# Performance work log

Measured on AMD Instinct MI355X. Metric: run time of the kernel, lower is better.

## Reference

```python
import jax, jax.numpy as jnp
import numpy as np
from jax import lax

T, H, F, E, K = 4096, 1024, 2048, 8, 2

def setup_inputs() -> dict:
    key = jax.random.key(0)
    k1, k2, k3, k4 = jax.random.split(key, 4)
    return {
        "hidden_states": jax.random.normal(k1, (T, H), jnp.float32),
        "gate_w": jax.random.normal(k2, (E, H), jnp.float32) * 0.02,
        "w1": jax.random.normal(k3, (E, 2 * F, H), jnp.float32) * 0.02,  # fused gate+up
        "w2": jax.random.normal(k4, (E, H, F), jnp.float32) * 0.02,      # down proj
        "top_k": K,
    }

def reference(hidden_states, gate_w, w1, w2, top_k):
    tokens = hidden_states.shape[0]
    # Router gate (Linear, no bias)
    router_logits = hidden_states @ gate_w.T                     # [T, E]
    probs = jax.nn.softmax(router_logits.astype(jnp.float32), axis=-1)
    topk_w, topk_idx = lax.top_k(probs, top_k)                   # [T, K]
    topk_w = topk_w / jnp.sum(topk_w, axis=-1, keepdims=True)    # renormalize
    # Dense combine weights [T, E] (zero for unselected experts)
    combine = jnp.zeros_like(probs).at[jnp.arange(tokens)[:, None], topk_idx].add(topk_w)
    combine = combine.astype(hidden_states.dtype)

    def expert_step(acc, ew):
        w1_e, w2_e, c_e = ew                                     # [2F,H], [H,F], [T]
        h = hidden_states @ w1_e.T                               # [T, 2F]
        g, u = jnp.split(h, 2, axis=-1)
        y = (jax.nn.silu(g) * u) @ w2_e.T                        # [T, H]
        return acc + c_e[:, None] * y, None

    acc0 = jnp.zeros_like(hidden_states)
    final_hidden_states, _ = lax.scan(expert_step, acc0, (w1, w2, combine.T))
    return final_hidden_states, router_logits
```

## Files before the change

### kernel.cpp

```cpp
#include <hip/hip_runtime.h>

#define T 4096
#define Hdim 1024
#define Fdim 2048
#define NE 8
#define TOPK 2
#define TK (T*TOPK)

typedef unsigned short ushort_t;
typedef __attribute__((ext_vector_type(8))) short bf16x8;
typedef __attribute__((ext_vector_type(4))) float floatx4;

__device__ __forceinline__ ushort_t f2bf(float f) {
    unsigned u = __float_as_uint(f);
    u += 0x7fff + ((u >> 16) & 1);
    return (ushort_t)(u >> 16);
}
__device__ __forceinline__ uint4 cvt8(const float4 a, const float4 b) {
    uint4 r;
    r.x = (unsigned)f2bf(a.x) | ((unsigned)f2bf(a.y) << 16);
    r.y = (unsigned)f2bf(a.z) | ((unsigned)f2bf(a.w) << 16);
    r.z = (unsigned)f2bf(b.x) | ((unsigned)f2bf(b.y) << 16);
    r.w = (unsigned)f2bf(b.z) | ((unsigned)f2bf(b.w) << 16);
    return r;
}
__device__ __forceinline__ void gld16(const ushort_t* g, short* l) {
    __builtin_amdgcn_global_load_lds((const __attribute__((address_space(1))) void*)g,
                                     (__attribute__((address_space(3))) void*)l, 16, 0, 0);
}

__global__ __launch_bounds__(256) void cvt_kernel(const float* __restrict__ src,
                                                  ushort_t* __restrict__ dst)
{
    long i = (long)blockIdx.x * 256 + threadIdx.x;
    float4 a = *(const float4*)(src + i * 8);
    float4 b = *(const float4*)(src + i * 8 + 4);
    *(uint4*)(dst + i * 8) = cvt8(a, b);
}

__global__ __launch_bounds__(64) void router_kernel(
    const float* __restrict__ hs, const float* __restrict__ gw,
    float* __restrict__ logits_out, ushort_t* __restrict__ hsb,
    int2* __restrict__ choice, float2* __restrict__ cwt, int* __restrict__ counts)
{
    const int t = blockIdx.x;
    const int lane = threadIdx.x;
    if (t == 0 && lane < NE) counts[lane] = 0;

    float hreg[16];
#pragma unroll
    for (int i = 0; i < 16; ++i)
        hreg[i] = hs[(long)t * Hdim + lane + 64 * i];

#pragma unroll
    for (int i = 0; i < 16; ++i)
        hsb[(long)t * Hdim + lane + 64 * i] = f2bf(hreg[i]);

    float acc[NE];
#pragma unroll
    for (int e = 0; e < NE; ++e) {
        float s = 0.f;
#pragma unroll
        for (int i = 0; i < 16; ++i)
            s += hreg[i] * gw[e * Hdim + lane + 64 * i];
#pragma unroll
        for (int off = 32; off > 0; off >>= 1)
            s += __shfl_xor(s, off, 64);
        acc[e] = s;
    }

    if (lane < NE) logits_out[t * NE + lane] = acc[lane];

    if (lane == 0) {
        int i1 = 0;
#pragma unroll
        for (int e = 1; e < NE; ++e) if (acc[e] > acc[i1]) i1 = e;
        int i2 = -1;
#pragma unroll
        for (int e = 0; e < NE; ++e) {
            if (e == i1) continue;
            if (i2 < 0 || acc[e] > acc[i2]) i2 = e;
        }
        float p2 = __expf(acc[i2] - acc[i1]);
        float z  = 1.f + p2;
        choice[t] = make_int2(i1, i2);
        cwt[t]    = make_float2(1.f / z, p2 / z);
    }
}

__global__ __launch_bounds__(256) void scatter_kernel(
    const int2* __restrict__ choice, const float2* __restrict__ cwt,
    int* __restrict__ counts, int* __restrict__ tok_slot, float* __restrict__ tok_wt)
{
    __shared__ int lhist[NE];
    __shared__ int lbase[NE];
    __shared__ int lpos[NE];
    const int tid = threadIdx.x;
    if (tid < NE) { lhist[tid] = 0; lpos[tid] = 0; }
    __syncthreads();

    const int t = blockIdx.x * 256 + tid;
    int2   ch = choice[t];
    float2 wv = cwt[t];
    atomicAdd(&lhist[ch.x], 1);
    atomicAdd(&lhist[ch.y], 1);
    __syncthreads();

    if (tid < NE) lbase[tid] = atomicAdd(&counts[tid], lhist[tid]);
    __syncthreads();

    int p1 = atomicAdd(&lpos[ch.x], 1);
    int p2 = atomicAdd(&lpos[ch.y], 1);
    int o1 = lbase[ch.x] + p1;
    int o2 = lbase[ch.y] + p2;
    tok_slot[ch.x * T + o1] = t * TOPK + 0;
    tok_wt [ch.x * T + o1] = wv.x;
    tok_slot[ch.y * T + o2] = t * TOPK + 1;
    tok_wt [ch.y * T + o2] = wv.y;
}

__global__ __launch_bounds__(512) void gemm1_kernel(
    const ushort_t* __restrict__ hsb, const ushort_t* __restrict__ w1b,
    const int* __restrict__ counts, const int* __restrict__ tok_slot,
    ushort_t* __restrict__ actb)
{
    const int e = blockIdx.z;
    const int cnt = counts[e];
    const int row0 = blockIdx.y * 256;
    if (row0 >= cnt) return;
    const int f0 = blockIdx.x * 128;

    __shared__ short As[2][256 * 64];
    __shared__ short Bs[2][256 * 64];
    __shared__ int slotLds[256];

    const int tid = threadIdx.x;
    if (tid < 256) {
        int idx = row0 + tid;
        slotLds[tid] = (idx < cnt) ? tok_slot[e * T + idx] : -1;
    }
    __syncthreads();

    const ushort_t* srcA[4];
    const ushort_t* srcB[4];
#pragma unroll
    for (int i = 0; i < 4; ++i) {
        int ci = i * 512 + tid;
        int r  = ci >> 3;
        int gc = (ci & 7) ^ (r & 7);
        int s  = slotLds[r];
        srcA[i] = hsb + (long)(s >= 0 ? (s >> 1) : 0) * Hdim + gc * 8;
        long frow = (r < 128) ? (long)(f0 + r) : (long)(Fdim + f0 + (r - 128));
        srcB[i] = w1b + ((long)e * 2 * Fdim + frow) * Hdim + gc * 8;
    }

    const int lane = tid & 63;
    const int w = tid >> 6;
    const int wm = (w >> 1) * 64;
    const int fn = (w & 1) * 64;
    const int fr = lane & 15, fg = lane >> 4;
    const int cs0 = (fg ^ (fr & 7)) * 8;
    const int cs1 = ((4 + fg) ^ (fr & 7)) * 8;

    floatx4 accg[4][4] = {};
    floatx4 accu[4][4] = {};

#pragma unroll
    for (int i = 0; i < 4; ++i) {
        gld16(srcA[i], &As[0][(i * 512 + tid) * 8]);
        gld16(srcB[i], &Bs[0][(i * 512 + tid) * 8]);
    }
    __syncthreads();

    const int NT = Hdim / 64;
    for (int t = 0; t < NT; ++t) {
        short* Ac = As[t & 1];
        short* Bc = Bs[t & 1];
        short* An = As[(t & 1) ^ 1];
        short* Bn = Bs[(t & 1) ^ 1];
        const bool pf = (t + 1 < NT);
        const long k1 = (long)(t + 1) * 64;

        bf16x8 a[4], b[4];

#pragma unroll
        for (int ms = 0; ms < 4; ++ms)
            a[ms] = *(const bf16x8*)&Ac[(wm + ms * 16 + fr) * 64 + cs0];
#pragma unroll
        for (int ns = 0; ns < 4; ++ns)
            b[ns] = *(const bf16x8*)&Bc[(fn + ns * 16 + fr) * 64 + cs0];
        if (pf) {
            gld16(srcA[0] + k1, &An[(0 * 512 + tid) * 8]);
            gld16(srcB[0] + k1, &Bn[(0 * 512 + tid) * 8]);
        }
        __builtin_amdgcn_s_barrier();
        __builtin_amdgcn_s_setprio(1);
#pragma unroll
        for (int ms = 0; ms < 4; ++ms)
#pragma unroll
            for (int ns = 0; ns < 4; ++ns)
                accg[ms][ns] = __builtin_amdgcn_mfma_f32_16x16x32_bf16(a[ms], b[ns], accg[ms][ns], 0, 0, 0);
        __builtin_amdgcn_s_setprio(0);
        __builtin_amdgcn_s_barrier();

#pragma unroll
        for (int ns = 0; ns < 4; ++ns)
            b[ns] = *(const bf16x8*)&Bc[(128 + fn + ns * 16 + fr) * 64 + cs0];
        if (pf) {
            gld16(srcA[1] + k1, &An[(1 * 512 + tid) * 8]);
            gld16(srcB[1] + k1, &Bn[(1 * 512 + tid) * 8]);
        }
        __builtin_amdgcn_s_barrier();
        __builtin_amdgcn_s_setprio(1);
#pragma unroll
        for (int ms = 0; ms < 4; ++ms)
#pragma unroll
            for (int ns = 0; ns < 4; ++ns)
                accu[ms][ns] = __builtin_amdgcn_mfma_f32_16x16x32_bf16(a[ms], b[ns], accu[ms][ns], 0, 0, 0);
        __builtin_amdgcn_s_setprio(0);
        __builtin_amdgcn_s_barrier();

#pragma unroll
        for (int ms = 0; ms < 4; ++ms)
            a[ms] = *(const bf16x8*)&Ac[(wm + ms * 16 + fr) * 64 + cs1];
#pragma unroll
        for (int ns = 0; ns < 4; ++ns)
            b[ns] = *(const bf16x8*)&Bc[(fn + ns * 16 + fr) * 64 + cs1];
        if (pf) {
            gld16(srcA[2] + k1, &An[(2 * 512 + tid) * 8]);
            gld16(srcB[2] + k1, &Bn[(2 * 512 + tid) * 8]);
        }
        __builtin_amdgcn_s_barrier();
        __builtin_amdgcn_s_setprio(1);
#pragma unroll
        for (int ms = 0; ms < 4; ++ms)
#pragma unroll
            for (int ns = 0; ns < 4; ++ns)
                accg[ms][ns] = __builtin_amdgcn_mfma_f32_16x16x32_bf16(a[ms], b[ns], accg[ms][ns], 0, 0, 0);
        __builtin_amdgcn_s_setprio(0);
        __builtin_amdgcn_s_barrier();

#pragma unroll
        for (int ns = 0; ns < 4; ++ns)
            b[ns] = *(const bf16x8*)&Bc[(128 + fn + ns * 16 + fr) * 64 + cs1];
        if (pf) {
            gld16(srcA[3] + k1, &An[(3 * 512 + tid) * 8]);
            gld16(srcB[3] + k1, &Bn[(3 * 512 + tid) * 8]);
        }
        __builtin_amdgcn_s_barrier();
        __builtin_amdgcn_s_setprio(1);
#pragma unroll
        for (int ms = 0; ms < 4; ++ms)
#pragma unroll
            for (int ns = 0; ns < 4; ++ns)
                accu[ms][ns] = __builtin_amdgcn_mfma_f32_16x16x32_bf16(a[ms], b[ns], accu[ms][ns], 0, 0, 0);
        __builtin_amdgcn_s_setprio(0);
        __builtin_amdgcn_sched_barrier(0);
        asm volatile("s_waitcnt vmcnt(0)" ::: "memory");
        __builtin_amdgcn_s_barrier();
    }

#pragma unroll
    for (int ms = 0; ms < 4; ++ms)
#pragma unroll
        for (int ns = 0; ns < 4; ++ns)
#pragma unroll
            for (int j = 0; j < 4; ++j) {
                int m = wm + ms * 16 + fg * 4 + j;
                int slot = slotLds[m];
                if (slot >= 0) {
                    int fcol = f0 + fn + ns * 16 + fr;
                    float gv = accg[ms][ns][j];
                    float uv = accu[ms][ns][j];
                    float av = (gv / (1.f + __expf(-gv))) * uv;
                    actb[(long)slot * Fdim + fcol] = f2bf(av);
                }
            }
}

__global__ __launch_bounds__(512) void gemm2_kernel(
    const ushort_t* __restrict__ actb, const ushort_t* __restrict__ w2b,
    const int* __restrict__ counts, const int* __restrict__ tok_slot,
    const float* __restrict__ tok_wt, float* __restrict__ partial)
{
    const int e = blockIdx.z;
    const int cnt = counts[e];
    const int row0 = blockIdx.y * 128;
    if (row0 >= cnt) return;
    const int h0 = blockIdx.x * 128;

    __shared__ short As[128 * 64];
    __shared__ short Bs[128 * 64];
    __shared__ int   slotLds[128];
    __shared__ float wtLds[128];

    const int tid = threadIdx.x;
    if (tid < 128) {
        int idx = row0 + tid;
        bool ok = idx < cnt;
        slotLds[tid] = ok ? tok_slot[e * T + idx] : -1;
        wtLds[tid]   = ok ? tok_wt [e * T + idx] : 0.f;
    }
    __syncthreads();

    const ushort_t* srcA[2];
    const ushort_t* srcB[2];
#pragma unroll
    for (int i = 0; i < 2; ++i) {
        int ci = i * 512 + tid;
        int r  = ci >> 3;
        int gc = (ci & 7) ^ (r & 7);
        int s  = slotLds[r];
        srcA[i] = actb + (long)(s >= 0 ? s : 0) * Fdim + gc * 8;
        srcB[i] = w2b + ((long)e * Hdim + (h0 + r)) * Fdim + gc * 8;
    }

    const int lane = tid & 63;
    const int w = tid >> 6;
    const int wm = (w >> 2) * 64;
    const int wn = (w & 3) * 32;
    const int fr = lane & 15, fg = lane >> 4;
    const int cs0 = (fg ^ (fr & 7)) * 8;
    const int cs1 = ((4 + fg) ^ (fr & 7)) * 8;

    floatx4 acc[4][2] = {};

    for (int k0 = 0; k0 < Fdim; k0 += 64) {
        __syncthreads();
        gld16(srcA[0] + k0, &As[tid * 8]);
        gld16(srcA[1] + k0, &As[(512 + tid) * 8]);
        gld16(srcB[0] + k0, &Bs[tid * 8]);
        gld16(srcB[1] + k0, &Bs[(512 + tid) * 8]);
        __syncthreads();

#pragma unroll
        for (int kk = 0; kk < 2; ++kk) {
            const int cs = kk ? cs1 : cs0;
            bf16x8 a[4], b[2];
#pragma unroll
            for (int ms = 0; ms < 4; ++ms)
                a[ms] = *(bf16x8*)&As[(wm + ms * 16 + fr) * 64 + cs];
#pragma unroll
            for (int ns = 0; ns < 2; ++ns)
                b[ns] = *(bf16x8*)&Bs[(wn + ns * 16 + fr) * 64 + cs];
#pragma unroll
            for (int ms = 0; ms < 4; ++ms)
#pragma unroll
                for (int ns = 0; ns < 2; ++ns)
                    acc[ms][ns] = __builtin_amdgcn_mfma_f32_16x16x32_bf16(a[ms], b[ns], acc[ms][ns], 0, 0, 0);
        }
    }

#pragma unroll
    for (int ms = 0; ms < 4; ++ms)
#pragma unroll
        for (int ns = 0; ns < 2; ++ns)
#pragma unroll
            for (int j = 0; j < 4; ++j) {
                int m = wm + ms * 16 + fg * 4 + j;
                int slot = slotLds[m];
                if (slot >= 0) {
                    int hcol = h0 + wn + ns * 16 + fr;
                    partial[(long)slot * Hdim + hcol] = acc[ms][ns][j] * wtLds[m];
                }
            }
}

__global__ __launch_bounds__(256) void combine_kernel(
    const float* __restrict__ partial, float* __restrict__ out)
{
    long i = (long)blockIdx.x * 256 + threadIdx.x;
    int t  = (int)(i / (Hdim / 4));
    int h4 = (int)(i % (Hdim / 4));
    const float4 p0 = *(const float4*)&partial[(long)(2 * t    ) * Hdim + h4 * 4];
    const float4 p1 = *(const float4*)&partial[(long)(2 * t + 1) * Hdim + h4 * 4];
    float4 s;
    s.x = p0.x + p1.x; s.y = p0.y + p1.y; s.z = p0.z + p1.z; s.w = p0.w + p1.w;
    *(float4*)&out[(long)t * Hdim + h4 * 4] = s;
}

extern "C" void kernel_launch(void* const* d_in, const int* in_sizes, int n_in,
                              void* d_out, int out_size, void* d_ws, size_t ws_size,
                              hipStream_t stream)
{
    const float* hs = (const float*)d_in[0];
    const float* gw = (const float*)d_in[1];
    const float* w1 = (const float*)d_in[2];
    const float* w2 = (const float*)d_in[3];

    float* out        = (float*)d_out;
    float* logits_out = out + (long)T * Hdim;

    char* ws = (char*)d_ws;
    size_t off = 0;
    int* counts = (int*)(ws + off);          off += 256;
    int* tok_slot = (int*)(ws + off);        off += (size_t)NE * T * sizeof(int);
    float* tok_wt = (float*)(ws + off);      off += (size_t)NE * T * sizeof(float);
    off = (off + 255) & ~(size_t)255;
    ushort_t* hsb = (ushort_t*)(ws + off);   off += (size_t)T * Hdim * sizeof(ushort_t);
    off = (off + 255) & ~(size_t)255;
    char* w1region = ws + off;               off += (size_t)NE * 2 * Fdim * Hdim * sizeof(ushort_t);
    ushort_t* w1b = (ushort_t*)w1region;
    ushort_t* w2b = (ushort_t*)w1region;
    float* partial = (float*)(w1region + (size_t)NE * Hdim * Fdim * sizeof(ushort_t));
    off = (off + 255) & ~(size_t)255;
    ushort_t* actb = (ushort_t*)(ws + off);  off += (size_t)TK * Fdim * sizeof(ushort_t);
    int2*   choice = (int2*)actb;
    float2* cwt    = (float2*)((char*)actb + (size_t)T * sizeof(int2));

    const long n8_w1 = (long)NE * 2 * Fdim * Hdim / 8;
    const long n8_w2 = (long)NE * Hdim * Fdim / 8;

    cvt_kernel<<<(int)(n8_w1 / 256), 256, 0, stream>>>(w1, w1b);
    router_kernel<<<T, 64, 0, stream>>>(hs, gw, logits_out, hsb, choice, cwt, counts);
    scatter_kernel<<<T / 256, 256, 0, stream>>>(choice, cwt, counts, tok_slot, tok_wt);
    gemm1_kernel<<<dim3(Fdim / 128, T / 256, NE), 512, 0, stream>>>(hsb, w1b, counts, tok_slot, actb);
    cvt_kernel<<<(int)(n8_w2 / 256), 256, 0, stream>>>(w2, w2b);
    gemm2_kernel<<<dim3(Hdim / 128, T / 128, NE), 512, 0, stream>>>(actb, w2b, counts, tok_slot, tok_wt, partial);
    combine_kernel<<<(int)((long)T * Hdim / 4 / 256), 256, 0, stream>>>(partial, out);
}
```

Baseline: 429.7 us.

## Triple-buffer gemm2 with 256-row tiles and regroup gemm1 prefetch waits

gemm2 moves from a single-buffered 128x128 tile with two full barriers per K step to a 256x128 tile with a three-stage LDS ring. Loads are issued two steps ahead and waited on with partial vmcnt counts, so global latency overlaps MFMA work and each B tile is reused across more rows. gemm1's prefetch is regrouped so all A loads go out in the first phase and all B loads in the second, with fine-grained vmcnt waits replacing the full drain at the end of each iteration. The cost is more LDS (about 144 KB in gemm2), which lowers occupancy, and correctness now depends on the hand-counted vmcnt values.

```diff
diff --git a/kernel.cpp b/kernel.cpp
--- a/kernel.cpp
+++ b/kernel.cpp
@@ -166,11 +166,11 @@
     floatx4 accu[4][4] = {};
 
 #pragma unroll
-    for (int i = 0; i < 4; ++i) {
-        gld16(srcA[i], &As[0][(i * 512 + tid) * 8]);
-        gld16(srcB[i], &Bs[0][(i * 512 + tid) * 8]);
-    }
-    __syncthreads();
+    for (int i = 0; i < 4; ++i) gld16(srcA[i], &As[0][(i * 512 + tid) * 8]);
+#pragma unroll
+    for (int i = 0; i < 4; ++i) gld16(srcB[i], &Bs[0][(i * 512 + tid) * 8]);
+    asm volatile("s_waitcnt vmcnt(2)" ::: "memory");
+    __builtin_amdgcn_s_barrier();
 
     const int NT = Hdim / 64;
     for (int t = 0; t < NT; ++t) {
@@ -190,8 +190,9 @@
         for (int ns = 0; ns < 4; ++ns)
             b[ns] = *(const bf16x8*)&Bc[(fn + ns * 16 + fr) * 64 + cs0];
         if (pf) {
-            gld16(srcA[0] + k1, &An[(0 * 512 + tid) * 8]);
-            gld16(srcB[0] + k1, &Bn[(0 * 512 + tid) * 8]);
+#pragma unroll
+            for (int i = 0; i < 4; ++i)
+                gld16(srcA[i] + k1, &An[(i * 512 + tid) * 8]);
         }
         __builtin_amdgcn_s_barrier();
         __builtin_amdgcn_s_setprio(1);
@@ -201,14 +202,17 @@
             for (int ns = 0; ns < 4; ++ns)
                 accg[ms][ns] = __builtin_amdgcn_mfma_f32_16x16x32_bf16(a[ms], b[ns], accg[ms][ns], 0, 0, 0);
         __builtin_amdgcn_s_setprio(0);
+        if (pf) asm volatile("s_waitcnt vmcnt(4)" ::: "memory");
+        else    asm volatile("s_waitcnt vmcnt(0)" ::: "memory");
         __builtin_amdgcn_s_barrier();
 
 #pragma unroll
         for (int ns = 0; ns < 4; ++ns)
             b[ns] = *(const bf16x8*)&Bc[(128 + fn + ns * 16 + fr) * 64 + cs0];
         if (pf) {
-            gld16(srcA[1] + k1, &An[(1 * 512 + tid) * 8]);
-            gld16(srcB[1] + k1, &Bn[(1 * 512 + tid) * 8]);
+#pragma unroll
+            for (int i = 0; i < 4; ++i)
+                gld16(srcB[i] + k1, &Bn[(i * 512 + tid) * 8]);
         }
         __builtin_amdgcn_s_barrier();
         __builtin_amdgcn_s_setprio(1);
@@ -226,10 +230,6 @@
 #pragma unroll
         for (int ns = 0; ns < 4; ++ns)
             b[ns] = *(const bf16x8*)&Bc[(fn + ns * 16 + fr) * 64 + cs1];
-        if (pf) {
-            gld16(srcA[2] + k1, &An[(2 * 512 + tid) * 8]);
-            gld16(srcB[2] + k1, &Bn[(2 * 512 + tid) * 8]);
-        }
         __builtin_amdgcn_s_barrier();
         __builtin_amdgcn_s_setprio(1);
 #pragma unroll
@@ -243,10 +243,6 @@
 #pragma unroll
         for (int ns = 0; ns < 4; ++ns)
             b[ns] = *(const bf16x8*)&Bc[(128 + fn + ns * 16 + fr) * 64 + cs1];
-        if (pf) {
-            gld16(srcA[3] + k1, &An[(3 * 512 + tid) * 8]);
-            gld16(srcB[3] + k1, &Bn[(3 * 512 + tid) * 8]);
-        }
         __builtin_amdgcn_s_barrier();
         __builtin_amdgcn_s_setprio(1);
 #pragma unroll
@@ -255,8 +251,7 @@
             for (int ns = 0; ns < 4; ++ns)
                 accu[ms][ns] = __builtin_amdgcn_mfma_f32_16x16x32_bf16(a[ms], b[ns], accu[ms][ns], 0, 0, 0);
         __builtin_amdgcn_s_setprio(0);
-        __builtin_amdgcn_sched_barrier(0);
-        asm volatile("s_waitcnt vmcnt(0)" ::: "memory");
+        if (pf) asm volatile("s_waitcnt vmcnt(2)" ::: "memory");
         __builtin_amdgcn_s_barrier();
     }
 
@@ -285,17 +280,17 @@
 {
     const int e = blockIdx.z;
     const int cnt = counts[e];
-    const int row0 = blockIdx.y * 128;
+    const int row0 = blockIdx.y * 256;
     if (row0 >= cnt) return;
     const int h0 = blockIdx.x * 128;
 
-    __shared__ short As[128 * 64];
-    __shared__ short Bs[128 * 64];
-    __shared__ int   slotLds[128];
-    __shared__ float wtLds[128];
+    __shared__ short As[3][256 * 64];
+    __shared__ short Bs[3][128 * 64];
+    __shared__ int   slotLds[256];
+    __shared__ float wtLds[256];
 
     const int tid = threadIdx.x;
-    if (tid < 128) {
+    if (tid < 256) {
         int idx = row0 + tid;
         bool ok = idx < cnt;
         slotLds[tid] = ok ? tok_slot[e * T + idx] : -1;
@@ -303,58 +298,111 @@
     }
     __syncthreads();
 
-    const ushort_t* srcA[2];
+    const ushort_t* srcA[4];
     const ushort_t* srcB[2];
 #pragma unroll
-    for (int i = 0; i < 2; ++i) {
+    for (int i = 0; i < 4; ++i) {
         int ci = i * 512 + tid;
         int r  = ci >> 3;
         int gc = (ci & 7) ^ (r & 7);
         int s  = slotLds[r];
         srcA[i] = actb + (long)(s >= 0 ? s : 0) * Fdim + gc * 8;
+    }
+#pragma unroll
+    for (int i = 0; i < 2; ++i) {
+        int ci = i * 512 + tid;
+        int r  = ci >> 3;
+        int gc = (ci & 7) ^ (r & 7);
         srcB[i] = w2b + ((long)e * Hdim + (h0 + r)) * Fdim + gc * 8;
     }
 
     const int lane = tid & 63;
     const int w = tid >> 6;
-    const int wm = (w >> 2) * 64;
-    const int wn = (w & 3) * 32;
+    const int wm = (w >> 1) * 64;
+    const int wn = (w & 1) * 64;
     const int fr = lane & 15, fg = lane >> 4;
     const int cs0 = (fg ^ (fr & 7)) * 8;
     const int cs1 = ((4 + fg) ^ (fr & 7)) * 8;
 
-    floatx4 acc[4][2] = {};
-
-    for (int k0 = 0; k0 < Fdim; k0 += 64) {
-        __syncthreads();
-        gld16(srcA[0] + k0, &As[tid * 8]);
-        gld16(srcA[1] + k0, &As[(512 + tid) * 8]);
-        gld16(srcB[0] + k0, &Bs[tid * 8]);
-        gld16(srcB[1] + k0, &Bs[(512 + tid) * 8]);
-        __syncthreads();
-
-#pragma unroll
-        for (int kk = 0; kk < 2; ++kk) {
-            const int cs = kk ? cs1 : cs0;
-            bf16x8 a[4], b[2];
-#pragma unroll
-            for (int ms = 0; ms < 4; ++ms)
-                a[ms] = *(bf16x8*)&As[(wm + ms * 16 + fr) * 64 + cs];
-#pragma unroll
-            for (int ns = 0; ns < 2; ++ns)
-                b[ns] = *(bf16x8*)&Bs[(wn + ns * 16 + fr) * 64 + cs];
-#pragma unroll
-            for (int ms = 0; ms < 4; ++ms)
-#pragma unroll
-                for (int ns = 0; ns < 2; ++ns)
-                    acc[ms][ns] = __builtin_amdgcn_mfma_f32_16x16x32_bf16(a[ms], b[ns], acc[ms][ns], 0, 0, 0);
-        }
+    floatx4 acc[4][4] = {};
+
+#pragma unroll
+    for (int i = 0; i < 4; ++i) gld16(srcA[i],      &As[0][(i * 512 + tid) * 8]);
+#pragma unroll
+    for (int i = 0; i < 2; ++i) gld16(srcB[i],      &Bs[0][(i * 512 + tid) * 8]);
+#pragma unroll
+    for (int i = 0; i < 4; ++i) gld16(srcA[i] + 64, &As[1][(i * 512 + tid) * 8]);
+#pragma unroll
+    for (int i = 0; i < 2; ++i) gld16(srcB[i] + 64, &Bs[1][(i * 512 + tid) * 8]);
+    asm volatile("s_waitcnt vmcnt(6)" ::: "memory");
+    __builtin_amdgcn_s_barrier();
+
+    const int NT = Fdim / 64;
+    int cur = 0;
+    for (int t = 0; t < NT; ++t) {
+        short* Ac = &As[cur][0];
+        short* Bc = &Bs[cur][0];
+        int stg = cur + 2; if (stg >= 3) stg -= 3;
+        short* Astg = &As[stg][0];
+        short* Bstg = &Bs[stg][0];
+        const bool pf2 = (t + 2 < NT);
+        const long k2 = (long)(t + 2) * 64;
+
+        bf16x8 a[4], b[4];
+
+#pragma unroll
+        for (int ms = 0; ms < 4; ++ms)
+            a[ms] = *(const bf16x8*)&Ac[(wm + ms * 16 + fr) * 64 + cs0];
+#pragma unroll
+        for (int ns = 0; ns < 4; ++ns)
+            b[ns] = *(const bf16x8*)&Bc[(wn + ns * 16 + fr) * 64 + cs0];
+        if (pf2) {
+#pragma unroll
+            for (int i = 0; i < 4; ++i)
+                gld16(srcA[i] + k2, &Astg[(i * 512 + tid) * 8]);
+        }
+        __builtin_amdgcn_s_barrier();
+        __builtin_amdgcn_s_setprio(1);
+#pragma unroll
+        for (int ms = 0; ms < 4; ++ms)
+#pragma unroll
+            for (int ns = 0; ns < 4; ++ns)
+                acc[ms][ns] = __builtin_amdgcn_mfma_f32_16x16x32_bf16(a[ms], b[ns], acc[ms][ns], 0, 0, 0);
+        __builtin_amdgcn_s_setprio(0);
+        __builtin_amdgcn_s_barrier();
+
+#pragma unroll
+        for (int ms = 0; ms < 4; ++ms)
+            a[ms] = *(const bf16x8*)&Ac[(wm + ms * 16 + fr) * 64 + cs1];
+#pragma unroll
+        for (int ns = 0; ns < 4; ++ns)
+            b[ns] = *(const bf16x8*)&Bc[(wn + ns * 16 + fr) * 64 + cs1];
+        if (pf2) {
+#pragma unroll
+            for (int i = 0; i < 2; ++i)
+                gld16(srcB[i] + k2, &Bstg[(i * 512 + tid) * 8]);
+        }
+        __builtin_amdgcn_s_barrier();
+        __builtin_amdgcn_s_setprio(1);
+#pragma unroll
+        for (int ms = 0; ms < 4; ++ms)
+#pragma unroll
+            for (int ns = 0; ns < 4; ++ns)
+                acc[ms][ns] = __builtin_amdgcn_mfma_f32_16x16x32_bf16(a[ms], b[ns], acc[ms][ns], 0, 0, 0);
+        __builtin_amdgcn_s_setprio(0);
+        if (t + 1 < NT) {
+            if (pf2) asm volatile("s_waitcnt vmcnt(6)" ::: "memory");
+            else     asm volatile("s_waitcnt vmcnt(0)" ::: "memory");
+        }
+        __builtin_amdgcn_s_barrier();
+
+        cur += 1; if (cur >= 3) cur -= 3;
     }
 
 #pragma unroll
     for (int ms = 0; ms < 4; ++ms)
 #pragma unroll
-        for (int ns = 0; ns < 2; ++ns)
+        for (int ns = 0; ns < 4; ++ns)
 #pragma unroll
             for (int j = 0; j < 4; ++j) {
                 int m = wm + ms * 16 + fg * 4 + j;
@@ -416,6 +464,6 @@
     scatter_kernel<<<T / 256, 256, 0, stream>>>(choice, cwt, counts, tok_slot, tok_wt);
     gemm1_kernel<<<dim3(Fdim / 128, T / 256, NE), 512, 0, stream>>>(hsb, w1b, counts, tok_slot, actb);
     cvt_kernel<<<(int)(n8_w2 / 256), 256, 0, stream>>>(w2, w2b);
-    gemm2_kernel<<<dim3(Hdim / 128, T / 128, NE), 512, 0, stream>>>(actb, w2b, counts, tok_slot, tok_wt, partial);
+    gemm2_kernel<<<dim3(Hdim / 128, T / 256, NE), 512, 0, stream>>>(actb, w2b, counts, tok_slot, tok_wt, partial);
     combine_kernel<<<(int)((long)T * Hdim / 4 / 256), 256, 0, stream>>>(partial, out);
 }
```

New measurement: 465.7 us. 8.4% more time.
